# Optimization experiments

Measured on AMD Instinct MI355X. Metric: run time of the kernel, lower is better.

Reference implementation:

```python
import jax, jax.numpy as jnp
import numpy as np

K = 20
EPS = 1e-5
NUM_CLASSES = 50


def knn_idx(x, k):
    # x: [B, C, N] -> [B, N, k] indices of k nearest neighbors (self included)
    xx = jnp.sum(x * x, axis=1)                      # [B, N]
    inner = jnp.einsum('bcn,bcm->bnm', x, x)         # [B, N, N]
    neg_dist = 2.0 * inner - xx[:, :, None] - xx[:, None, :]
    return jax.lax.top_k(neg_dist, k)[1]


def graph_feature(x, k):
    # x: [B, C, N] -> [B, 2C, N, k] edge features (feat - center, center)
    B = x.shape[0]
    idx = knn_idx(x, k)                              # [B, N, k]
    xt = jnp.transpose(x, (0, 2, 1))                 # [B, N, C]
    feat = xt[jnp.arange(B)[:, None, None], idx]     # [B, N, k, C]
    center = xt[:, :, None, :]
    out = jnp.concatenate([feat - center, jnp.broadcast_to(center, feat.shape)], axis=-1)
    return jnp.transpose(out, (0, 3, 1, 2))


def group_norm(x, groups, w, b):
    B, C = x.shape[0], x.shape[1]
    shp = x.shape
    xg = x.reshape(B, groups, -1)
    mu = jnp.mean(xg, axis=-1, keepdims=True)
    var = jnp.var(xg, axis=-1, keepdims=True)
    xn = ((xg - mu) * jax.lax.rsqrt(var + EPS)).reshape(shp)
    bshape = (1, C) + (1,) * (len(shp) - 2)
    return xn * w.reshape(bshape) + b.reshape(bshape)


def leaky(x):
    return jnp.where(x >= 0, x, 0.2 * x)


def edge_block(x, W, gw, gb, groups, k):
    f = graph_feature(x, k)                          # [B, 2C, N, k]
    h = jnp.einsum('oc,bcnk->bonk', W, f)            # 1x1 conv2d, no bias
    h = leaky(group_norm(h, groups, gw, gb))
    return jnp.max(h, axis=-1)                       # [B, Cout, N]


def conv1d(x, W, b):
    return jnp.einsum('oc,bcn->bon', W, x) + b[None, :, None]


def _mk(key, shape, fan_in):
    return jax.random.normal(key, shape, jnp.float32) * (1.0 / np.sqrt(fan_in))


def setup_inputs():
    key = jax.random.key(0)
    ks = jax.random.split(key, 32)
    B, N = 8, 2048
    d = {}
    d['x'] = jax.random.normal(ks[0], (B, 3, N), jnp.float32)
    d['W1'] = _mk(ks[1], (64, 6), 6)
    d['W2'] = _mk(ks[2], (64, 128), 128)
    d['W3'] = _mk(ks[3], (128, 128), 128)
    for i, (name, c) in enumerate([('g1', 64), ('g2', 64), ('g3', 128), ('gf', 1024), ('gs1', 512), ('gs2', 256), ('gs3', 128)]):
        d[name + 'w'] = 1.0 + 0.02 * jax.random.normal(ks[4 + 2 * i], (c,), jnp.float32)
        d[name + 'b'] = 0.02 * jax.random.normal(ks[5 + 2 * i], (c,), jnp.float32)
    d['Wm'] = _mk(ks[20], (1024, 256), 256)
    d['bm'] = jnp.zeros((1024,), jnp.float32)
    d['Ws1'] = _mk(ks[21], (512, 1280), 1280)
    d['bs1'] = jnp.zeros((512,), jnp.float32)
    d['Ws2'] = _mk(ks[22], (256, 512), 512)
    d['bs2'] = jnp.zeros((256,), jnp.float32)
    d['Ws3'] = _mk(ks[23], (128, 256), 256)
    d['bs3'] = jnp.zeros((128,), jnp.float32)
    d['Ws4'] = _mk(ks[24], (NUM_CLASSES, 128), 128)
    d['bs4'] = jnp.zeros((NUM_CLASSES,), jnp.float32)
    return d


def reference(x, W1, W2, W3, g1w, g1b, g2w, g2b, g3w, g3b, gfw, gfb, gs1w, gs1b, gs2w, gs2b, gs3w, gs3b, Wm, bm, Ws1, bs1, Ws2, bs2, Ws3, bs3, Ws4, bs4):
    B, _, N = x.shape
    x1 = edge_block(x, W1, g1w, g1b, 8, K)           # [B, 64, N]
    x2 = edge_block(x1, W2, g2w, g2b, 8, K)          # [B, 64, N]
    x3 = edge_block(x2, W3, g3w, g3b, 8, K)          # [B, 128, N]
    feats = jnp.concatenate([x1, x2, x3], axis=1)    # [B, 256, N]
    xb = jax.nn.relu(group_norm(conv1d(feats, Wm, bm), 32, gfw, gfb))  # [B, 1024, N]
    xmax = jnp.max(xb, axis=2)                       # [B, 1024]
    xmax_exp = jnp.broadcast_to(xmax[:, :, None], (B, 1024, N))
    combined = jnp.concatenate([xmax_exp, feats], axis=1)  # [B, 1280, N]
    h = jax.nn.relu(group_norm(conv1d(combined, Ws1, bs1), 16, gs1w, gs1b))
    h = jax.nn.relu(group_norm(conv1d(h, Ws2, bs2), 16, gs2w, gs2b))
    h = jax.nn.relu(group_norm(conv1d(h, Ws3, bs3), 8, gs3w, gs3b))
    logits = conv1d(h, Ws4, bs4)                     # [B, num_classes, N]
    return jax.nn.log_softmax(logits, axis=1)
```

## Files before the change

### kernel.cpp

```cpp
#include <hip/hip_runtime.h>

#define BN 8
#define NP 2048
#define KK 20
#define EPSV 1e-5f

typedef __attribute__((ext_vector_type(8))) short bf16x8;
typedef __attribute__((ext_vector_type(4))) float f32x4;

static __device__ __forceinline__ float leakyf(float v){ return v >= 0.f ? v : 0.2f*v; }
static __device__ __forceinline__ unsigned fenc(float f){
  unsigned u = __float_as_uint(f);
  unsigned m = (unsigned)((int)u >> 31);
  return u ^ (m | 0x80000000u);
}
static __device__ __forceinline__ float fdec(unsigned u){
  return __uint_as_float((u & 0x80000000u) ? (u & 0x7FFFFFFFu) : ~u);
}
static __device__ __forceinline__ unsigned bf2(float a, float b){
  unsigned ua = __float_as_uint(a), ub = __float_as_uint(b);
  ua = (ua + 0x7FFFu + ((ua>>16)&1u)) >> 16;
  ub = (ub + 0x7FFFu + ((ub>>16)&1u)) >> 16;
  return ua | (ub<<16);
}
static __device__ __forceinline__ unsigned short b16(float v){
  unsigned u = __float_as_uint(v);
  return (unsigned short)((u + 0x7FFFu + ((u>>16)&1u)) >> 16);
}
static __device__ __forceinline__ unsigned umax32(unsigned a, unsigned b){ return __builtin_elementwise_max(a,b); }
static __device__ __forceinline__ unsigned med3u(unsigned a, unsigned b, unsigned c){
  unsigned d;
  asm("v_med3_u32 %0, %1, %2, %3" : "=v"(d) : "v"(a), "v"(b), "v"(c));
  return d;
}

static __device__ __forceinline__ char* ldsW(char* base, int row, int colb){
  return base + row*80 + (colb ^ ((((unsigned)row>>3)&3u)<<4));
}
static __device__ __forceinline__ char* ldsX(char* base, int row, int colb){
  return base + row*80 + (colb ^ (((((unsigned)row>>2)^((unsigned)row>>4))&3u)<<4));
}
static __device__ __forceinline__ int swz128(int row, int colb){
  return (colb ^ ((row&7)<<4));
}

__global__ __launch_bounds__(256) void xx_kernel(const float* __restrict__ x, long ldb, int C,
                                                 float* __restrict__ xx){
  int b = blockIdx.y;
  int n = blockIdx.x*256 + threadIdx.x;
  const float* xp = x + (long)b*ldb + n;
  float a = 0.f;
  for(int c=0;c<C;c++){ float v = xp[(long)c*NP]; a += v*v; }
  xx[b*NP + n] = a;
}

static __device__ __forceinline__ void ins20(unsigned* tv, unsigned key){
  unsigned pold = tv[0];
  tv[0] = umax32(tv[0], key);
  #pragma unroll
  for(int r=1;r<20;r++){
    unsigned cold = tv[r];
    tv[r] = med3u(key, pold, cold);
    pold = cold;
  }
}

__global__ __launch_bounds__(256) void knnf_kernel(const unsigned short* __restrict__ fh,
                                                   const unsigned short* __restrict__ fl,
                                                   const float* __restrict__ xx,
                                                   unsigned* __restrict__ pk){
  __shared__ unsigned SK[64][68];
  const int b    = blockIdx.z;
  const int part = blockIdx.y;
  const int q0   = blockIdx.x*64;
  const int t    = threadIdx.x;
  const int lane = t & 63;
  const int w    = t >> 6;
  const int lr   = lane & 15, lg = lane >> 4;
  const unsigned short* fhb = fh + (long)b*NP*64;
  const unsigned short* flb = fl + (long)b*NP*64;
  const float* xxb = xx + b*NP;

  const unsigned short* qa = fhb + ((long)(q0 + w*16 + lr))*64 + lg*8;
  const unsigned short* qb = flb + ((long)(q0 + w*16 + lr))*64 + lg*8;
  bf16x8 ah0 = *(const bf16x8*)(qa);
  bf16x8 ah1 = *(const bf16x8*)(qa + 32);
  bf16x8 al0 = *(const bf16x8*)(qb);
  bf16x8 al1 = *(const bf16x8*)(qb + 32);
  float4 qxx4 = *(const float4*)(xxb + q0 + w*16 + lg*4);
  float qxx[4] = {qxx4.x, qxx4.y, qxx4.z, qxx4.w};

  unsigned tv[20];
  #pragma unroll
  for(int r=0;r<20;r++) tv[r] = 0u;
  const int sq = t>>2, sl = t&3;

  bf16x8 F[16];
  float cx[4];
  {
    const int ct = part*4;
    #pragma unroll
    for(int nt=0;nt<4;nt++){
      const unsigned short* ca = fhb + ((long)(ct*64 + nt*16 + lr))*64 + lg*8;
      const unsigned short* cb = flb + ((long)(ct*64 + nt*16 + lr))*64 + lg*8;
      F[nt*4+0] = *(const bf16x8*)(ca);
      F[nt*4+1] = *(const bf16x8*)(ca + 32);
      F[nt*4+2] = *(const bf16x8*)(cb);
      F[nt*4+3] = *(const bf16x8*)(cb + 32);
      cx[nt] = xxb[ct*64 + nt*16 + lr];
    }
  }

  #pragma unroll
  for(int cc=0; cc<4; cc++){
    __builtin_amdgcn_s_setprio(1);
    f32x4 acc[4];
    #pragma unroll
    for(int nt=0; nt<4; nt++){
      f32x4 a = (f32x4){0.f,0.f,0.f,0.f};
      a = __builtin_amdgcn_mfma_f32_16x16x32_bf16(ah0, F[nt*4+0], a, 0,0,0);
      a = __builtin_amdgcn_mfma_f32_16x16x32_bf16(ah1, F[nt*4+1], a, 0,0,0);
      a = __builtin_amdgcn_mfma_f32_16x16x32_bf16(ah0, F[nt*4+2], a, 0,0,0);
      a = __builtin_amdgcn_mfma_f32_16x16x32_bf16(ah1, F[nt*4+3], a, 0,0,0);
      a = __builtin_amdgcn_mfma_f32_16x16x32_bf16(al0, F[nt*4+0], a, 0,0,0);
      a = __builtin_amdgcn_mfma_f32_16x16x32_bf16(al1, F[nt*4+1], a, 0,0,0);
      acc[nt] = a;
    }
    __builtin_amdgcn_s_setprio(0);
    unsigned key4[4][4];
    #pragma unroll
    for(int nt=0; nt<4; nt++){
      #pragma unroll
      for(int r=0;r<4;r++){
        float neg = 2.f*acc[nt][r] - qxx[r] - cx[nt];
        key4[nt][r] = (fenc(neg) & 0xFFFFFF00u) | (255u - (unsigned)(cc*64 + nt*16 + lr));
      }
    }
    __syncthreads();
    #pragma unroll
    for(int nt=0; nt<4; nt++)
      #pragma unroll
      for(int r=0;r<4;r++)
        SK[w*16 + lg*4 + r][nt*16 + lr] = key4[nt][r];
    __syncthreads();
    if (cc < 3){
      const int ct = part*4 + cc + 1;
      #pragma unroll
      for(int nt=0;nt<4;nt++){
        const unsigned short* ca = fhb + ((long)(ct*64 + nt*16 + lr))*64 + lg*8;
        const unsigned short* cb = flb + ((long)(ct*64 + nt*16 + lr))*64 + lg*8;
        F[nt*4+0] = *(const bf16x8*)(ca);
        F[nt*4+1] = *(const bf16x8*)(ca + 32);
        F[nt*4+2] = *(const bf16x8*)(cb);
        F[nt*4+3] = *(const bf16x8*)(cb + 32);
        cx[nt] = xxb[ct*64 + nt*16 + lr];
      }
    }
    __builtin_amdgcn_sched_barrier(0);
    #pragma unroll
    for(int jj=0;jj<4;jj++){
      uint4 kv = *(const uint4*)&SK[sq][sl*16 + jj*4];
      ins20(tv, kv.x); ins20(tv, kv.y); ins20(tv, kv.z); ins20(tv, kv.w);
    }
  }
  long base = ((((long)b*NP + q0 + sq)*8 + part)*4 + sl)*20;
  #pragma unroll
  for(int r=0;r<20;r++) pk[base+r] = tv[r];
}

__global__ __launch_bounds__(256) void knn1_kernel(const float* __restrict__ x,
                                                   const float* __restrict__ xx,
                                                   unsigned* __restrict__ pk){
  __shared__ float cx0[256], cx1[256], cx2[256], cxxa[256];
  const int b    = blockIdx.z;
  const int part = blockIdx.y;
  const int q0   = blockIdx.x*64;
  const int t    = threadIdx.x;
  const float* xb  = x + (long)b*3*NP;
  const float* xxb = xx + b*NP;

  cx0[t]  = xb[part*256 + t];
  cx1[t]  = xb[NP + part*256 + t];
  cx2[t]  = xb[2*NP + part*256 + t];
  cxxa[t] = xxb[part*256 + t];

  const int sq = t>>2, sl = t&3;
  const int q = q0 + sq;
  float qx = xb[q], qy = xb[NP + q], qz = xb[2*NP + q];
  float qxx = xxb[q];
  __syncthreads();

  unsigned tv[20];
  #pragma unroll
  for(int r=0;r<20;r++) tv[r] = 0u;

  for(int cc=0; cc<4; cc++){
    #pragma unroll
    for(int j=0;j<16;j++){
      int m = cc*64 + sl*16 + j;
      float ip = qx*cx0[m] + qy*cx1[m] + qz*cx2[m];
      float neg = 2.f*ip - qxx - cxxa[m];
      unsigned key = (fenc(neg) & 0xFFFFFF00u) | (255u - (unsigned)m);
      ins20(tv, key);
    }
  }
  long base = ((((long)b*NP + q0 + sq)*8 + part)*4 + sl)*20;
  #pragma unroll
  for(int r=0;r<20;r++) pk[base+r] = tv[r];
}

__global__ __launch_bounds__(256) void knnmerge_kernel(const unsigned* __restrict__ pk,
                                                       int* __restrict__ idxout){
  const int wid  = threadIdx.x >> 6;
  const int lane = threadIdx.x & 63;
  const long qg = (long)blockIdx.x*4 + wid;
  const unsigned* kb = pk + qg*640;
  const int l = lane >> 1, h = lane & 1;
  unsigned k[10];
  {
    const unsigned* src = kb + l*20 + h*10;
    #pragma unroll
    for(int i=0;i<10;i++) k[i] = src[i];
  }
  int rem = 10;
  int* op = idxout + qg*KK;
  const int gbase = (l>>2)*256;
  for(int r=0;r<KK;r++){
    unsigned key = k[0];
    int gi = gbase + 255 - (int)(key & 255u);
    unsigned long long cmp = (rem > 0)
        ? ((unsigned long long)(key & 0xFFFFFF00u) << 32) | (unsigned)(0x7FFFFFFF - gi)
        : 0ull;
    unsigned long long w = cmp;
    #pragma unroll
    for(int s=1;s<64;s<<=1){
      unsigned long long o = __shfl_xor(w, s, 64);
      w = (o > w) ? o : w;
    }
    if (lane == 0){
      op[r] = 0x7FFFFFFF - (int)(unsigned)(w & 0xFFFFFFFFu);
    }
    if (cmp == w){
      #pragma unroll
      for(int i=0;i<9;i++) k[i] = k[i+1];
      rem--;
    }
  }
}

template<int CIN, int O>
__global__ __launch_bounds__(256) void pcdual_kernel(const float* __restrict__ x, long ldb,
                                                     const float* __restrict__ W,
                                                     float* __restrict__ ya, float* __restrict__ dd){
  __shared__ float Wt[CIN][O+1];
  constexpr int NLOC = 256/O;
  const int b = blockIdx.y;
  const int n0 = blockIdx.x*NLOC;
  const int t = threadIdx.x;
  const int o = t % O;
  const int n = n0 + t/O;
  const float* xp = x + (long)b*ldb + n;
  float xv[CIN];
  #pragma unroll
  for(int c=0;c<CIN;c++) xv[c] = xp[(long)c*NP];
  for(int i=t;i<CIN*O;i+=256){ int oo=i/CIN, c=i%CIN; Wt[c][oo] = W[(long)oo*2*CIN + c]; }
  __syncthreads();
  float aa = 0.f;
  #pragma unroll
  for(int c=0;c<CIN;c++) aa += Wt[c][o]*xv[c];
  __syncthreads();
  for(int i=t;i<CIN*O;i+=256){ int oo=i/CIN, c=i%CIN; Wt[c][oo] = W[(long)oo*2*CIN + CIN + c]; }
  __syncthreads();
  float ab = 0.f;
  #pragma unroll
  for(int c=0;c<CIN;c++) ab += Wt[c][o]*xv[c];
  long outoff = ((long)b*NP + n)*O + o;
  ya[outoff] = aa;
  dd[outoff] = ab - aa;
}

template<int O>
__global__ __launch_bounds__(256) void pcdualm_kernel(const unsigned short* __restrict__ fh,
                                                      const unsigned short* __restrict__ fl,
                                                      const float* __restrict__ W,
                                                      float* __restrict__ ya, float* __restrict__ dd){
  __shared__ unsigned short AH[O][64];
  __shared__ unsigned short AL[O][64];
  __shared__ unsigned short DH[O][64];
  __shared__ unsigned short DL[O][64];
  const int b  = blockIdx.y;
  const int n0 = blockIdx.x*64;
  const int t  = threadIdx.x;
  const int lane = t & 63;
  const int w  = t >> 6;
  const int lr = lane & 15, lg = lane >> 4;

  for(int i=t; i<O*64; i+=256){
    int o = i >> 6, c = i & 63;
    float va = W[(long)o*128 + c];
    float vb = W[(long)o*128 + 64 + c];
    float vd = vb - va;
    unsigned short ah = b16(va);
    unsigned short dh = b16(vd);
    int byt = swz128(o, c*2);
    *(unsigned short*)((char*)&AH[o][0] + byt) = ah;
    *(unsigned short*)((char*)&AL[o][0] + byt) = b16(va - __uint_as_float(((unsigned)ah)<<16));
    *(unsigned short*)((char*)&DH[o][0] + byt) = dh;
    *(unsigned short*)((char*)&DL[o][0] + byt) = b16(vd - __uint_as_float(((unsigned)dh)<<16));
  }

  const int n = n0 + w*16 + lr;
  const unsigned short* xh = fh + ((long)b*NP + n)*64 + lg*8;
  const unsigned short* xl = fl + ((long)b*NP + n)*64 + lg*8;
  bf16x8 xh0 = *(const bf16x8*)(xh);
  bf16x8 xh1 = *(const bf16x8*)(xh + 32);
  bf16x8 xl0 = *(const bf16x8*)(xl);
  bf16x8 xl1 = *(const bf16x8*)(xl + 32);
  __syncthreads();

  #pragma unroll
  for(int mi=0; mi<O/16; mi++){
    int row = mi*16 + lr;
    bf16x8 a_h0 = *(const bf16x8*)((char*)&AH[row][0] + swz128(row, lg*16));
    bf16x8 a_h1 = *(const bf16x8*)((char*)&AH[row][0] + swz128(row, 64 + lg*16));
    bf16x8 a_l0 = *(const bf16x8*)((char*)&AL[row][0] + swz128(row, lg*16));
    bf16x8 a_l1 = *(const bf16x8*)((char*)&AL[row][0] + swz128(row, 64 + lg*16));
    f32x4 aa = (f32x4){0.f,0.f,0.f,0.f};
    aa = __builtin_amdgcn_mfma_f32_16x16x32_bf16(a_h0, xh0, aa, 0,0,0);
    aa = __builtin_amdgcn_mfma_f32_16x16x32_bf16(a_h1, xh1, aa, 0,0,0);
    aa = __builtin_amdgcn_mfma_f32_16x16x32_bf16(a_h0, xl0, aa, 0,0,0);
    aa = __builtin_amdgcn_mfma_f32_16x16x32_bf16(a_h1, xl1, aa, 0,0,0);
    aa = __builtin_amdgcn_mfma_f32_16x16x32_bf16(a_l0, xh0, aa, 0,0,0);
    aa = __builtin_amdgcn_mfma_f32_16x16x32_bf16(a_l1, xh1, aa, 0,0,0);
    bf16x8 d_h0 = *(const bf16x8*)((char*)&DH[row][0] + swz128(row, lg*16));
    bf16x8 d_h1 = *(const bf16x8*)((char*)&DH[row][0] + swz128(row, 64 + lg*16));
    bf16x8 d_l0 = *(const bf16x8*)((char*)&DL[row][0] + swz128(row, lg*16));
    bf16x8 d_l1 = *(const bf16x8*)((char*)&DL[row][0] + swz128(row, 64 + lg*16));
    f32x4 ad = (f32x4){0.f,0.f,0.f,0.f};
    ad = __builtin_amdgcn_mfma_f32_16x16x32_bf16(d_h0, xh0, ad, 0,0,0);
    ad = __builtin_amdgcn_mfma_f32_16x16x32_bf16(d_h1, xh1, ad, 0,0,0);
    ad = __builtin_amdgcn_mfma_f32_16x16x32_bf16(d_h0, xl0, ad, 0,0,0);
    ad = __builtin_amdgcn_mfma_f32_16x16x32_bf16(d_h1, xl1, ad, 0,0,0);
    ad = __builtin_amdgcn_mfma_f32_16x16x32_bf16(d_l0, xh0, ad, 0,0,0);
    ad = __builtin_amdgcn_mfma_f32_16x16x32_bf16(d_l1, xh1, ad, 0,0,0);
    long ooff = ((long)b*NP + n)*O + mi*16 + lg*4;
    float4 va = {aa[0],aa[1],aa[2],aa[3]};
    float4 vd = {ad[0],ad[1],ad[2],ad[3]};
    *(float4*)(ya + ooff) = va;
    *(float4*)(dd + ooff) = vd;
  }
}

template<int O>
__global__ __launch_bounds__(256) void egather_kernel(const float* __restrict__ ya, const float* __restrict__ dd,
                               const int* __restrict__ idx,
                               float* __restrict__ mx, float* __restrict__ mn,
                               float* __restrict__ stats){
  __shared__ float sred2[4][16];
  constexpr int NSUB = 256/O;
  constexpr int CPG = O/8;
  const int b  = blockIdx.x & 7;
  const int n0 = (blockIdx.x >> 3) * 32;
  const int t = threadIdx.x;
  const int w = t >> 6;
  const int o = t % O;
  const int ns = t / O;
  if (t < 64) sred2[t>>4][t&15] = 0.f;
  __syncthreads();
  float gs = 0.f, gs2 = 0.f;
  const float* yab = ya + (long)b*NP*O;
  for(int p=ns; p<32; p+=NSUB){
    int n = n0 + p;
    float d = dd[((long)b*NP + n)*O + o];
    const int* ip = idx + ((long)b*NP + n)*KK;
    float m = -__builtin_inff(), mm = __builtin_inff(), s = 0.f, s2 = 0.f;
    #pragma unroll
    for(int k=0;k<KK;k++){
      int j = ip[k];
      float v = yab[(long)j*O + o] + d;
      s += v; s2 += v*v;
      m = fmaxf(m, v); mm = fminf(mm, v);
    }
    mx[((long)b*NP + n)*O + o] = m;
    mn[((long)b*NP + n)*O + o] = mm;
    gs += s; gs2 += s2;
  }
  #pragma unroll
  for(int offm=1; offm<CPG; offm<<=1){
    gs  += __shfl_xor(gs,  offm, CPG);
    gs2 += __shfl_xor(gs2, offm, CPG);
  }
  if ((o & (CPG-1)) == 0){
    int g = o / CPG;
    sred2[w][g*2]   = gs;
    sred2[w][g*2+1] = gs2;
  }
  __syncthreads();
  if (t < 16){
    float a = sred2[0][t] + sred2[1][t] + sred2[2][t] + sred2[3][t];
    atomicAdd(&stats[b*16 + t], a);
  }
}

template<int O, bool NEEDXX, bool WRITEH>
__global__ __launch_bounds__(256) void enorm_kernel(const float* __restrict__ mx, const float* __restrict__ mn,
                                                    const float* __restrict__ stats,
                                                    const float* __restrict__ gw, const float* __restrict__ gb,
                                                    float* __restrict__ feats, int coff,
                                                    float* __restrict__ xxout,
                                                    unsigned* __restrict__ fhout, unsigned* __restrict__ flout){
  __shared__ float lmx[64][65];
  __shared__ float lmn[64][65];
  const int b = blockIdx.z;
  const int o0 = blockIdx.y*64;
  const int n0 = blockIdx.x*64;
  const int t = threadIdx.x;
  for(int r=0;r<16;r++){
    int i = r*4 + t/64, j = t%64;
    long src = ((long)b*NP + n0 + i)*O + o0 + j;
    lmx[i][j] = mx[src];
    lmn[i][j] = mn[src];
  }
  __syncthreads();
  constexpr int CPG = O/8;
  const float inv_cnt = 1.f/((float)CPG*NP*KK);
  float xacc = 0.f;
  for(int r=0;r<16;r++){
    int ol = r*4 + t/64, nl = t%64;
    int og = o0 + ol;
    int g = og / CPG;
    float S  = stats[(b*8+g)*2];
    float S2 = stats[(b*8+g)*2+1];
    float mu = S*inv_cnt;
    float var = S2*inv_cnt - mu*mu;
    float rs = rsqrtf(var + EPSV);
    float w = gw[og], bb = gb[og];
    float sel = (w >= 0.f) ? lmx[nl][ol] : lmn[nl][ol];
    float v = leakyf((sel - mu)*rs*w + bb);
    feats[((long)b*256 + coff + og)*NP + n0 + nl] = v;
    if (WRITEH) lmx[nl][ol] = v;
    if (NEEDXX) xacc += v*v;
  }
  if (WRITEH){
    __syncthreads();
    #pragma unroll
    for(int k=0;k<8;k++){
      int flat = k*256 + t;
      int n = flat >> 5, cp = flat & 31;
      float v0 = lmx[n][2*cp], v1 = lmx[n][2*cp+1];
      unsigned short h0 = b16(v0), h1 = b16(v1);
      float r0 = v0 - __uint_as_float(((unsigned)h0)<<16);
      float r1 = v1 - __uint_as_float(((unsigned)h1)<<16);
      unsigned short l0 = b16(r0), l1 = b16(r1);
      long o = ((long)b*NP + n0 + n)*32 + cp;
      fhout[o] = (unsigned)h0 | ((unsigned)h1<<16);
      flout[o] = (unsigned)l0 | ((unsigned)l1<<16);
    }
  }
  if (NEEDXX){
    __syncthreads();
    float* red = &lmx[0][0];
    red[(t>>6)*64 + (t&63)] = xacc;
    __syncthreads();
    if (t < 64){
      float a = red[t] + red[64+t] + red[128+t] + red[192+t];
      xxout[b*NP + n0 + t] = a;
    }
  }
}

template<bool WRITE_Y, bool DO_STATS, bool DO_MAXMIN, bool IN_NORM>
__global__ __launch_bounds__(256) void mgemm_kernel(
    const float* __restrict__ W, int ldw,
    const float* __restrict__ x, long xldb,
    const float* __restrict__ bias, const float* __restrict__ basev,
    int O, int C, int gshift,
    float* __restrict__ y, float* __restrict__ stats,
    unsigned* __restrict__ mmax, unsigned* __restrict__ mmin,
    const float* __restrict__ instats, const float* __restrict__ igw,
    const float* __restrict__ igb, int igshift, float iinv)
{
  __shared__ __align__(16) char WlB[128*80];
  __shared__ __align__(16) char XtB[128*80];
  __shared__ float sred[16];
  __shared__ unsigned smax[128];
  __shared__ unsigned smin[128];

  const int b  = blockIdx.z;
  const int o0 = blockIdx.y*128;
  const int nb = blockIdx.x*128;
  const int t  = threadIdx.x;
  const int lane = t & 63;
  const int wid = t >> 6;
  const int wmo = wid >> 1, wno = wid & 1;
  const int lr = lane & 15, lg = lane >> 4;

  if (DO_STATS && t < 16) sred[t] = 0.f;
  if (DO_MAXMIN && t < 128){ smax[t] = 0u; smin[t] = 0xFFFFFFFFu; }

  f32x4 acc[4][4];
  #pragma unroll
  for(int i=0;i<4;i++)
    #pragma unroll
    for(int j=0;j<4;j++) acc[i][j] = (f32x4){0.f,0.f,0.f,0.f};

  const int so  = t & 127;
  const int scb = (t >> 7) << 5;
  const int xcg = t >> 5;
  const int xng = t & 31;

  for(int cc=0; cc<C; cc+=32){
    __syncthreads();
    {
      const float* wp = W + (long)(o0 + so)*ldw + cc + (scb>>1);
      #pragma unroll
      for(int j=0;j<4;j++){
        float4 f = *(const float4*)(wp + j*4);
        uint2 v = { bf2(f.x,f.y), bf2(f.z,f.w) };
        *(uint2*)ldsW(WlB, so, scb + j*8) = v;
      }
    }
    {
      const float* xp = x + (long)b*xldb + (long)(cc + xcg*4)*NP + nb + xng*4;
      float4 f0 = *(const float4*)(xp);
      float4 f1 = *(const float4*)(xp + NP);
      float4 f2 = *(const float4*)(xp + 2*NP);
      float4 f3 = *(const float4*)(xp + 3*NP);
      float X4[4][4] = {{f0.x,f0.y,f0.z,f0.w},{f1.x,f1.y,f1.z,f1.w},
                        {f2.x,f2.y,f2.z,f2.w},{f3.x,f3.y,f3.z,f3.w}};
      if (IN_NORM){
        #pragma unroll
        for(int i=0;i<4;i++){
          int c = cc + xcg*4 + i;
          int g = c >> igshift;
          const float* sp = instats + ((long)b*(C>>igshift) + g)*2;
          float mu = sp[0]*iinv;
          float var = sp[1]*iinv - mu*mu;
          float rs = rsqrtf(var + EPSV);
          float aa = rs*igw[c];
          float c2 = igb[c] - mu*aa;
          #pragma unroll
          for(int j=0;j<4;j++) X4[i][j] = fmaxf(X4[i][j]*aa + c2, 0.f);
        }
      }
      #pragma unroll
      for(int j=0;j<4;j++){
        uint2 v = { bf2(X4[0][j], X4[1][j]), bf2(X4[2][j], X4[3][j]) };
        *(uint2*)ldsX(XtB, xng*4 + j, xcg*8) = v;
      }
    }
    __syncthreads();
    bf16x8 afr[4], bfr[4];
    #pragma unroll
    for(int mi=0;mi<4;mi++) afr[mi] = *(const bf16x8*)ldsW(WlB, wmo*64 + mi*16 + lr, lg*16);
    #pragma unroll
    for(int nj=0;nj<4;nj++) bfr[nj] = *(const bf16x8*)ldsX(XtB, wno*64 + nj*16 + lr, lg*16);
    #pragma unroll
    for(int mi=0;mi<4;mi++)
      #pragma unroll
      for(int nj=0;nj<4;nj++)
        acc[mi][nj] = __builtin_amdgcn_mfma_f32_16x16x32_bf16(afr[mi], bfr[nj], acc[mi][nj], 0, 0, 0);
  }

  float bb4[4][4];
  #pragma unroll
  for(int mi=0;mi<4;mi++){
    #pragma unroll
    for(int r=0;r<4;r++){
      int o = o0 + wmo*64 + mi*16 + lg*4 + r;
      float v = 0.f;
      if (bias)  v += bias[o];
      if (basev) v += basev[(long)b*O + o];
      bb4[mi][r] = v;
    }
  }
  #pragma unroll
  for(int mi=0;mi<4;mi++)
    #pragma unroll
    for(int nj=0;nj<4;nj++)
      #pragma unroll
      for(int r=0;r<4;r++) acc[mi][nj][r] += bb4[mi][r];

  if (WRITE_Y){
    #pragma unroll
    for(int mi=0;mi<4;mi++)
      #pragma unroll
      for(int nj=0;nj<4;nj++)
        #pragma unroll
        for(int r=0;r<4;r++){
          int o = o0 + wmo*64 + mi*16 + lg*4 + r;
          y[((long)b*O + o)*NP + nb + wno*64 + nj*16 + lr] = acc[mi][nj][r];
        }
  }
  if (DO_STATS){
    #pragma unroll
    for(int mi=0;mi<4;mi++){
      float s = 0.f, s2 = 0.f;
      #pragma unroll
      for(int nj=0;nj<4;nj++)
        #pragma unroll
        for(int r=0;r<4;r++){ float v = acc[mi][nj][r]; s += v; s2 += v*v; }
      int gi = (wmo*64 + mi*16) >> gshift;
      atomicAdd(&sred[gi*2],   s);
      atomicAdd(&sred[gi*2+1], s2);
    }
  }
  if (DO_MAXMIN){
    #pragma unroll
    for(int mi=0;mi<4;mi++)
      #pragma unroll
      for(int r=0;r<4;r++){
        float mv = acc[mi][0][r], mw = acc[mi][0][r];
        #pragma unroll
        for(int nj=1;nj<4;nj++){ mv = fmaxf(mv, acc[mi][nj][r]); mw = fminf(mw, acc[mi][nj][r]); }
        int ol = wmo*64 + mi*16 + lg*4 + r;
        atomicMax(&smax[ol], fenc(mv));
        atomicMin(&smin[ol], fenc(mw));
      }
  }
  if (DO_STATS || DO_MAXMIN) __syncthreads();
  if (DO_STATS){
    int ngb = 128 >> gshift;
    if (t < ngb*2){
      atomicAdd(&stats[((long)b*(O>>gshift) + (o0>>gshift) + (t>>1))*2 + (t&1)], sred[t]);
    }
  }
  if (DO_MAXMIN){
    if (t < 128){
      atomicMax(&mmax[(long)b*O + o0 + t], smax[t]);
      atomicMin(&mmin[(long)b*O + o0 + t], smin[t]);
    }
  }
}

__global__ void xmax_kernel(const unsigned* __restrict__ mmax, const unsigned* __restrict__ mmin,
                            const float* __restrict__ stats, const float* __restrict__ gw,
                            const float* __restrict__ gb, float* __restrict__ xmax){
  int t = blockIdx.x*256 + threadIdx.x;
  int b = t >> 10, o = t & 1023;
  int g = o >> 5;
  const float* sp = stats + (b*32+g)*2;
  const float inv_cnt = 1.f/(32.f*NP);
  float mu = sp[0]*inv_cnt;
  float var = sp[1]*inv_cnt - mu*mu;
  float rs = rsqrtf(var + EPSV);
  float w = gw[o];
  float sel = (w >= 0.f) ? fdec(mmax[t]) : fdec(mmin[t]);
  float v = (sel - mu)*rs*w + gb[o];
  xmax[t] = fmaxf(v, 0.f);
}

__global__ __launch_bounds__(256) void base1_kernel(const float* __restrict__ Ws1, const float* __restrict__ bs1,
                                                    const float* __restrict__ xmax, float* __restrict__ base1){
  __shared__ float sred[4][8];
  const int o = blockIdx.x;
  const int t = threadIdx.x;
  const float* wp = Ws1 + (long)o*1280;
  float acc[8];
  #pragma unroll
  for(int bb=0;bb<8;bb++) acc[bb]=0.f;
  #pragma unroll
  for(int cc=0;cc<4;cc++){
    int c = cc*256 + t;
    float w = wp[c];
    #pragma unroll
    for(int bb=0;bb<8;bb++) acc[bb] += w * xmax[bb*1024 + c];
  }
  #pragma unroll
  for(int bb=0;bb<8;bb++){
    float a = acc[bb];
    a += __shfl_xor(a,1);  a += __shfl_xor(a,2);  a += __shfl_xor(a,4);
    a += __shfl_xor(a,8);  a += __shfl_xor(a,16); a += __shfl_xor(a,32);
    acc[bb]=a;
  }
  if ((t&63)==0){
    #pragma unroll
    for(int bb=0;bb<8;bb++) sred[t>>6][bb]=acc[bb];
  }
  __syncthreads();
  if (t<8){
    float a = sred[0][t]+sred[1][t]+sred[2][t]+sred[3][t] + bs1[o];
    base1[t*512 + o] = a;
  }
}

__global__ __launch_bounds__(256) void s4_kernel(const float* __restrict__ h3raw,
                                                 const float* __restrict__ stats,
                                                 const float* __restrict__ gw, const float* __restrict__ gb,
                                                 const float* __restrict__ W,
                                                 const float* __restrict__ bias,
                                                 float* __restrict__ out){
  const int b = blockIdx.y;
  const int n = blockIdx.x*64 + (threadIdx.x>>2);
  const int cl = threadIdx.x & 3;
  const float inv_cnt = 1.f/(16.f*NP);
  float mu0, rs0, mu1, rs1;
  {
    const float* sp = stats + (b*8 + cl*2)*2;
    mu0 = sp[0]*inv_cnt;
    float var = sp[1]*inv_cnt - mu0*mu0;
    rs0 = rsqrtf(var + EPSV);
    const float* sp1 = stats + (b*8 + cl*2 + 1)*2;
    mu1 = sp1[0]*inv_cnt;
    float var1 = sp1[1]*inv_cnt - mu1*mu1;
    rs1 = rsqrtf(var1 + EPSV);
  }
  float hv[32];
  #pragma unroll
  for(int c=0;c<32;c++){
    int og = cl*32 + c;
    float rs = (c < 16) ? rs0 : rs1;
    float mu = (c < 16) ? mu0 : mu1;
    float a = rs*gw[og];
    float c2 = gb[og] - mu*a;
    float v = h3raw[((long)b*128 + og)*NP + n];
    hv[c] = fmaxf(v*a + c2, 0.f);
  }
  float zz[50];
  #pragma unroll
  for(int o=0;o<50;o++){
    const float* wp = W + o*128 + cl*32;
    float a = 0.f;
    #pragma unroll
    for(int c=0;c<32;c++) a += wp[c]*hv[c];
    a += __shfl_xor(a,1);
    a += __shfl_xor(a,2);
    zz[o] = a + bias[o];
  }
  float m = zz[0];
  #pragma unroll
  for(int o=1;o<50;o++) m = fmaxf(m, zz[o]);
  float s = 0.f;
  #pragma unroll
  for(int o=0;o<50;o++) s += __expf(zz[o]-m);
  float lse = m + __logf(s);
  #pragma unroll
  for(int o=0;o<50;o++){
    if ((o&3)==cl) out[((long)b*50+o)*NP+n] = zz[o]-lse;
  }
}

extern "C" void kernel_launch(void* const* d_in, const int* in_sizes, int n_in,
                              void* d_out, int out_size, void* d_ws, size_t ws_size,
                              hipStream_t stream)
{
  const float* x   = (const float*)d_in[0];
  const float* W1  = (const float*)d_in[1];
  const float* W2  = (const float*)d_in[2];
  const float* W3  = (const float*)d_in[3];
  const float* g1w = (const float*)d_in[4];
  const float* g1b = (const float*)d_in[5];
  const float* g2w = (const float*)d_in[6];
  const float* g2b = (const float*)d_in[7];
  const float* g3w = (const float*)d_in[8];
  const float* g3b = (const float*)d_in[9];
  const float* gfw = (const float*)d_in[10];
  const float* gfb = (const float*)d_in[11];
  const float* gs1w= (const float*)d_in[12];
  const float* gs1b= (const float*)d_in[13];
  const float* gs2w= (const float*)d_in[14];
  const float* gs2b= (const float*)d_in[15];
  const float* gs3w= (const float*)d_in[16];
  const float* gs3b= (const float*)d_in[17];
  const float* Wm  = (const float*)d_in[18];
  const float* bm  = (const float*)d_in[19];
  const float* Ws1 = (const float*)d_in[20];
  const float* bs1 = (const float*)d_in[21];
  const float* Ws2 = (const float*)d_in[22];
  const float* bs2 = (const float*)d_in[23];
  const float* Ws3 = (const float*)d_in[24];
  const float* bs3 = (const float*)d_in[25];
  const float* Ws4 = (const float*)d_in[26];
  const float* bs4 = (const float*)d_in[27];
  float* out = (float*)d_out;

  char* ws = (char*)d_ws;
  size_t off = 0;
  auto alloc = [&](size_t bytes)->char*{
    char* p = ws + off;
    off += (bytes + 255) & ~(size_t)255;
    return p;
  };
  char* zbase = alloc(6656 + 32768);
  float* estats1 = (float*)(zbase + 0);
  float* estats2 = (float*)(zbase + 512);
  float* estats3 = (float*)(zbase + 1024);
  float* mstats  = (float*)(zbase + 1536);
  float* s1stats = (float*)(zbase + 3584);
  float* s2stats = (float*)(zbase + 4608);
  float* s3stats = (float*)(zbase + 5632);
  unsigned* mmax = (unsigned*)(zbase + 6656);
  unsigned* mmin = (unsigned*)alloc(32768);
  float* xmaxb = (float*)alloc(8*1024*4);
  float* base1 = (float*)alloc(8*512*4);
  float* feats = (float*)alloc((size_t)BN*256*NP*4);
  int*   idxb  = (int*)  alloc((size_t)BN*NP*KK*4);
  float* xxb   = (float*)alloc((size_t)BN*NP*4);
  unsigned* fhb = (unsigned*)alloc((size_t)BN*NP*64*2);
  unsigned* flb = (unsigned*)alloc((size_t)BN*NP*64*2);
  float* ya    = (float*)alloc((size_t)BN*NP*128*4);
  float* dd    = (float*)alloc((size_t)BN*NP*128*4);
  float* mx    = (float*)alloc((size_t)BN*NP*128*4);
  float* mn    = (float*)alloc((size_t)BN*NP*128*4);
  float* ybuf1 = (float*)alloc((size_t)BN*512*NP*4);
  float* ybuf2 = (float*)alloc((size_t)BN*256*NP*4);
  float* ybuf3 = (float*)alloc((size_t)BN*128*NP*4);

  unsigned* pk = (unsigned*)ya;
  const unsigned short* fh16 = (const unsigned short*)fhb;
  const unsigned short* fl16 = (const unsigned short*)flb;

  hipMemsetAsync(zbase, 0, 6656 + 32768, stream);
  hipMemsetAsync(mmin, 0xFF, 32768, stream);

  dim3 blk256(256);

  xx_kernel<<<dim3(NP/256, BN), blk256, 0, stream>>>(x, (long)3*NP, 3, xxb);
  knn1_kernel<<<dim3(NP/64, 8, BN), blk256, 0, stream>>>(x, xxb, pk);
  knnmerge_kernel<<<dim3(BN*NP/4), blk256, 0, stream>>>(pk, idxb);
  pcdual_kernel<3,64><<<dim3(NP/4, BN), blk256, 0, stream>>>(x, (long)3*NP, W1, ya, dd);
  egather_kernel<64><<<dim3(8*NP/32), blk256, 0, stream>>>(ya, dd, idxb, mx, mn, estats1);
  enorm_kernel<64,true,true><<<dim3(NP/64, 1, BN), blk256, 0, stream>>>(
      mx, mn, estats1, g1w, g1b, feats, 0, xxb, fhb, flb);

  knnf_kernel<<<dim3(NP/64, 8, BN), blk256, 0, stream>>>(fh16, fl16, xxb, pk);
  knnmerge_kernel<<<dim3(BN*NP/4), blk256, 0, stream>>>(pk, idxb);
  pcdualm_kernel<64><<<dim3(NP/64, BN), blk256, 0, stream>>>(fh16, fl16, W2, ya, dd);
  egather_kernel<64><<<dim3(8*NP/32), blk256, 0, stream>>>(ya, dd, idxb, mx, mn, estats2);
  enorm_kernel<64,true,true><<<dim3(NP/64, 1, BN), blk256, 0, stream>>>(
      mx, mn, estats2, g2w, g2b, feats, 64, xxb, fhb, flb);

  knnf_kernel<<<dim3(NP/64, 8, BN), blk256, 0, stream>>>(fh16, fl16, xxb, pk);
  knnmerge_kernel<<<dim3(BN*NP/4), blk256, 0, stream>>>(pk, idxb);
  pcdualm_kernel<128><<<dim3(NP/64, BN), blk256, 0, stream>>>(fh16, fl16, W3, ya, dd);
  egather_kernel<128><<<dim3(8*NP/32), blk256, 0, stream>>>(ya, dd, idxb, mx, mn, estats3);
  enorm_kernel<128,false,false><<<dim3(NP/64, 2, BN), blk256, 0, stream>>>(
      mx, mn, estats3, g3w, g3b, feats, 128, nullptr, nullptr, nullptr);

  mgemm_kernel<false,true,true,false><<<dim3(16,8,BN), blk256, 0, stream>>>(
      Wm, 256, feats, (long)256*NP, bm, nullptr, 1024, 256, 5,
      nullptr, mstats, mmax, mmin, nullptr, nullptr, nullptr, 0, 0.f);
  xmax_kernel<<<dim3(32), blk256, 0, stream>>>(mmax, mmin, mstats, gfw, gfb, xmaxb);
  base1_kernel<<<dim3(512), blk256, 0, stream>>>(Ws1, bs1, xmaxb, base1);

  mgemm_kernel<true,true,false,false><<<dim3(16,4,BN), blk256, 0, stream>>>(
      Ws1 + 1024, 1280, feats, (long)256*NP, nullptr, base1, 512, 256, 5,
      ybuf1, s1stats, nullptr, nullptr, nullptr, nullptr, nullptr, 0, 0.f);

  mgemm_kernel<true,true,false,true><<<dim3(16,2,BN), blk256, 0, stream>>>(
      Ws2, 512, ybuf1, (long)512*NP, bs2, nullptr, 256, 512, 4,
      ybuf2, s2stats, nullptr, nullptr, s1stats, gs1w, gs1b, 5, 1.f/(32.f*NP));

  mgemm_kernel<true,true,false,true><<<dim3(16,1,BN), blk256, 0, stream>>>(
      Ws3, 256, ybuf2, (long)256*NP, bs3, nullptr, 128, 256, 4,
      ybuf3, s3stats, nullptr, nullptr, s2stats, gs2w, gs2b, 4, 1.f/(16.f*NP));

  s4_kernel<<<dim3(NP/64, BN), blk256, 0, stream>>>(ybuf3, s3stats, gs3w, gs3b, Ws4, bs4, out);
}
```

Measured before the change: 603.4 us.

## Stage kNN candidate tiles cooperatively through shared memory instead of per-wave registers

Candidate feature tiles (high and low bf16 halves plus squared norms) are now loaded once per block into padded LDS arrays and read by each wave before its MFMAs. Previously every wave loaded the whole tile from global memory into a 16-entry bf16x8 register array. The goal is to cut redundant global traffic and free many VGPRs for better occupancy. In exchange, the next tile's global loads now complete before the barrier instead of overlapping the top-20 insertion work. The 136-byte LDS row pitch also leaves the 16-byte vector accesses misaligned.

```diff
diff --git a/kernel.cpp b/kernel.cpp
--- a/kernel.cpp
+++ b/kernel.cpp
@@ -69,7 +69,10 @@
                                                    const unsigned short* __restrict__ fl,
                                                    const float* __restrict__ xx,
                                                    unsigned* __restrict__ pk){
+  __shared__ unsigned short CH[64][68];
+  __shared__ unsigned short CL[64][68];
   __shared__ unsigned SK[64][68];
+  __shared__ float cxs[64];
   const int b    = blockIdx.z;
   const int part = blockIdx.y;
   const int q0   = blockIdx.x*64;
@@ -95,21 +98,20 @@
   for(int r=0;r<20;r++) tv[r] = 0u;
   const int sq = t>>2, sl = t&3;
 
-  bf16x8 F[16];
-  float cx[4];
-  {
-    const int ct = part*4;
-    #pragma unroll
-    for(int nt=0;nt<4;nt++){
-      const unsigned short* ca = fhb + ((long)(ct*64 + nt*16 + lr))*64 + lg*8;
-      const unsigned short* cb = flb + ((long)(ct*64 + nt*16 + lr))*64 + lg*8;
-      F[nt*4+0] = *(const bf16x8*)(ca);
-      F[nt*4+1] = *(const bf16x8*)(ca + 32);
-      F[nt*4+2] = *(const bf16x8*)(cb);
-      F[nt*4+3] = *(const bf16x8*)(cb + 32);
-      cx[nt] = xxb[ct*64 + nt*16 + lr];
-    }
-  }
+  #define STAGE(ct_)                                                                  \
+    {                                                                                 \
+      const int ct__ = (ct_);                                                         \
+      _Pragma("unroll")                                                               \
+      for(int i = t; i < 512; i += 256){                                              \
+        int row = i >> 3, seg = i & 7;                                                \
+        *(uint4*)&CH[row][seg*8] = *(const uint4*)(fhb + ((long)(ct__*64+row))*64 + seg*8); \
+        *(uint4*)&CL[row][seg*8] = *(const uint4*)(flb + ((long)(ct__*64+row))*64 + seg*8); \
+      }                                                                               \
+      if (t < 64) cxs[t] = xxb[ct__*64 + t];                                          \
+    }
+
+  STAGE(part*4);
+  __syncthreads();
 
   #pragma unroll
   for(int cc=0; cc<4; cc++){
@@ -117,22 +119,30 @@
     f32x4 acc[4];
     #pragma unroll
     for(int nt=0; nt<4; nt++){
+      int crow = nt*16 + lr;
+      bf16x8 bh0 = *(const bf16x8*)&CH[crow][lg*8];
+      bf16x8 bh1 = *(const bf16x8*)&CH[crow][32 + lg*8];
+      bf16x8 bl0 = *(const bf16x8*)&CL[crow][lg*8];
+      bf16x8 bl1 = *(const bf16x8*)&CL[crow][32 + lg*8];
       f32x4 a = (f32x4){0.f,0.f,0.f,0.f};
-      a = __builtin_amdgcn_mfma_f32_16x16x32_bf16(ah0, F[nt*4+0], a, 0,0,0);
-      a = __builtin_amdgcn_mfma_f32_16x16x32_bf16(ah1, F[nt*4+1], a, 0,0,0);
-      a = __builtin_amdgcn_mfma_f32_16x16x32_bf16(ah0, F[nt*4+2], a, 0,0,0);
-      a = __builtin_amdgcn_mfma_f32_16x16x32_bf16(ah1, F[nt*4+3], a, 0,0,0);
-      a = __builtin_amdgcn_mfma_f32_16x16x32_bf16(al0, F[nt*4+0], a, 0,0,0);
-      a = __builtin_amdgcn_mfma_f32_16x16x32_bf16(al1, F[nt*4+1], a, 0,0,0);
+      a = __builtin_amdgcn_mfma_f32_16x16x32_bf16(ah0, bh0, a, 0,0,0);
+      a = __builtin_amdgcn_mfma_f32_16x16x32_bf16(ah1, bh1, a, 0,0,0);
+      a = __builtin_amdgcn_mfma_f32_16x16x32_bf16(ah0, bl0, a, 0,0,0);
+      a = __builtin_amdgcn_mfma_f32_16x16x32_bf16(ah1, bl1, a, 0,0,0);
+      a = __builtin_amdgcn_mfma_f32_16x16x32_bf16(al0, bh0, a, 0,0,0);
+      a = __builtin_amdgcn_mfma_f32_16x16x32_bf16(al1, bh1, a, 0,0,0);
       acc[nt] = a;
     }
     __builtin_amdgcn_s_setprio(0);
+    float cxv[4];
+    #pragma unroll
+    for(int nt=0; nt<4; nt++) cxv[nt] = cxs[nt*16 + lr];
     unsigned key4[4][4];
     #pragma unroll
     for(int nt=0; nt<4; nt++){
       #pragma unroll
       for(int r=0;r<4;r++){
-        float neg = 2.f*acc[nt][r] - qxx[r] - cx[nt];
+        float neg = 2.f*acc[nt][r] - qxx[r] - cxv[nt];
         key4[nt][r] = (fenc(neg) & 0xFFFFFF00u) | (255u - (unsigned)(cc*64 + nt*16 + lr));
       }
     }
@@ -142,27 +152,17 @@
       #pragma unroll
       for(int r=0;r<4;r++)
         SK[w*16 + lg*4 + r][nt*16 + lr] = key4[nt][r];
+    if (cc < 3){
+      STAGE(part*4 + cc + 1);
+    }
     __syncthreads();
-    if (cc < 3){
-      const int ct = part*4 + cc + 1;
-      #pragma unroll
-      for(int nt=0;nt<4;nt++){
-        const unsigned short* ca = fhb + ((long)(ct*64 + nt*16 + lr))*64 + lg*8;
-        const unsigned short* cb = flb + ((long)(ct*64 + nt*16 + lr))*64 + lg*8;
-        F[nt*4+0] = *(const bf16x8*)(ca);
-        F[nt*4+1] = *(const bf16x8*)(ca + 32);
-        F[nt*4+2] = *(const bf16x8*)(cb);
-        F[nt*4+3] = *(const bf16x8*)(cb + 32);
-        cx[nt] = xxb[ct*64 + nt*16 + lr];
-      }
-    }
-    __builtin_amdgcn_sched_barrier(0);
     #pragma unroll
     for(int jj=0;jj<4;jj++){
       uint4 kv = *(const uint4*)&SK[sq][sl*16 + jj*4];
       ins20(tv, kv.x); ins20(tv, kv.y); ins20(tv, kv.z); ins20(tv, kv.w);
     }
   }
+  #undef STAGE
   long base = ((((long)b*NP + q0 + sq)*8 + part)*4 + sl)*20;
   #pragma unroll
   for(int r=0;r<20;r++) pk[base+r] = tv[r];
```

New measurement: 535.9 us, median of 2. 11.2% less time.
